# Optimization experiments

Measured on AMD Instinct MI355X. Metric: run time of the kernel, lower is better.

## Reference

```python
import jax, jax.numpy as jnp
import numpy as np

RADIUS = 0.05
HMIN = -0.02
HMAX = 0.04
NSAMPLE = 64


def setup_inputs() -> dict:
    key = jax.random.key(0)
    k1, k2, k3, k4 = jax.random.split(key, 4)
    B, N, P, C = 2, 16384, 1024, 256
    xyz = jax.random.uniform(k1, (B, N, 3), dtype=jnp.float32)
    new_xyz = jax.random.uniform(k2, (B, P, 3), dtype=jnp.float32)
    rot = jax.random.normal(k3, (B, P, 3, 3), dtype=jnp.float32)
    features = jax.random.normal(k4, (B, C, N), dtype=jnp.float32)
    return {"xyz": xyz, "new_xyz": new_xyz, "rot": rot, "features": features}


def cylinder_query(xyz, new_xyz, rot):
    """Returns (B, P, NSAMPLE) int32 indices into the N axis of xyz.

    Faithful to the torch version: the torch code sorts all N candidates by
    distance (knn with K=N) and then top-k's a cylinder score over them; since
    the candidate set is all N points, this equals a direct top-k of the score
    over N (candidate ordering only affects float ties).
    """
    # delta = candidate point - center, in world frame: (B, P, N, 3)
    delta = xyz[:, None, :, :] - new_xyz[:, :, None, :]
    # rotate into cylinder frame: matmul(delta, rot^T) -> sum_d delta_d * rot[j, d]
    dcyl = jnp.einsum('bpnd,bpjd->bpnj', delta, rot)
    x, y, z = dcyl[..., 0], dcyl[..., 1], dcyl[..., 2]
    radial = jnp.sqrt(jnp.maximum(y * y + z * z, 0.0))
    in_cyl = (radial <= RADIUS) & (x >= HMIN) & (x <= HMAX)
    score = jnp.where(in_cyl, radial + 1e-3 * jnp.abs(x), jnp.inf)
    # smallest-score top-k via top_k on negated score
    neg_vals, pos = jax.lax.top_k(-score, NSAMPLE)  # (B, P, NSAMPLE)
    vals = -neg_vals
    # fallback: nearest point (torch uses idx_cand[..., 0], the KNN-nearest)
    d2 = jnp.sum(delta * delta, axis=-1)  # (B, P, N)
    fallback = jnp.argmin(d2, axis=-1)  # (B, P)
    no_valid = jnp.isinf(vals[..., 0])  # no point inside cylinder
    idx = jnp.where(no_valid[..., None], fallback[..., None], pos)
    return idx


def reference(xyz, new_xyz, rot, features):
    B = xyz.shape[0]
    idx = cylinder_query(xyz, new_xyz, rot)  # (B, P, S)
    # group xyz: (B, P, S, 3)
    grouped_xyz = jax.vmap(lambda p, i: p[i])(xyz, idx)
    grouped_xyz = grouped_xyz - new_xyz[:, :, None, :]
    # rotate_xyz: grouped @ rot  -> sum_d g_d * rot[d, e]
    grouped_xyz = jnp.einsum('bpsd,bpde->bpse', grouped_xyz, rot)
    grouped_xyz = jnp.transpose(grouped_xyz, (0, 3, 1, 2))  # (B, 3, P, S)
    # group features: (B, C, P, S)
    grouped_feat = jax.vmap(lambda f, i: f[:, i])(features, idx)
    return jnp.concatenate([grouped_xyz, grouped_feat], axis=1)  # (B, 3+C, P, S)
```

## Files before the change

kernel.cpp:

```cpp
#include <hip/hip_runtime.h>
#include <stdint.h>

#define B_ 2
#define N_ 16384
#define P_ 1024
#define C_ 256
#define S_ 64
#define CH_ (C_ + 3)
#define CAP_ 512

#define INF_BITS 0x7F800000u

typedef unsigned long long u64;

struct QS {
    u64 keys[CAP_];
    uint32_t hist[4][256];
    u64 red[4];
    uint32_t wsum[4];
    int vflag[128];
    int cnt;
    int sel;
    uint32_t k;
};

struct GT {
    float tile[C_][33];
};

union USmem {
    QS qs;
    GT g;
};

__device__ __forceinline__ u64 umin64(u64 a, u64 b) { return a < b ? a : b; }

__device__ __forceinline__ uint32_t f2bf(float f) {
    uint32_t x = __float_as_uint(f);
    return (x + 0x7fffu + ((x >> 16) & 1u)) >> 16;
}
__device__ __forceinline__ float bf2f(uint32_t u) { return __uint_as_float(u << 16); }

__device__ u64 block_min_u64(u64 v, u64* s_red) {
    int tid = threadIdx.x;
#pragma unroll
    for (int o = 32; o > 0; o >>= 1)
        v = umin64(v, (u64)__shfl_xor(v, o, 64));
    __syncthreads();
    if ((tid & 63) == 0) s_red[tid >> 6] = v;
    __syncthreads();
    u64 r = s_red[0];
#pragma unroll
    for (int w = 1; w < 4; ++w) r = umin64(r, s_red[w]);
    return r;
}

__device__ __forceinline__ uint32_t eval_sb(float px, float py, float pz,
                                            float cx, float cy, float cz,
                                            float r0, float r1, float r2,
                                            float r3, float r4, float r5,
                                            float r6, float r7, float r8) {
    float dx = px - cx, dy = py - cy, dz = pz - cz;
    float xr = __fadd_rn(__fadd_rn(__fmul_rn(dx, r0), __fmul_rn(dy, r1)), __fmul_rn(dz, r2));
    float yr = __fadd_rn(__fadd_rn(__fmul_rn(dx, r3), __fmul_rn(dy, r4)), __fmul_rn(dz, r5));
    float zr = __fadd_rn(__fadd_rn(__fmul_rn(dx, r6), __fmul_rn(dy, r7)), __fmul_rn(dz, r8));
    float rad2 = __fadd_rn(__fmul_rn(yr, yr), __fmul_rn(zr, zr));
    float radial = __fsqrt_rn(fmaxf(rad2, 0.0f));
    bool valid = (radial <= 0.05f) && (xr >= -0.02f) && (xr <= 0.04f);
    float score = __fadd_rn(radial, __fmul_rn(1e-3f, fabsf(xr)));
    return valid ? __float_as_uint(score) : INF_BITS;
}

__device__ __forceinline__ uint32_t score_bits(const float* __restrict__ xb, int n,
                                               float cx, float cy, float cz,
                                               float r0, float r1, float r2,
                                               float r3, float r4, float r5,
                                               float r6, float r7, float r8) {
    return eval_sb(xb[n * 3 + 0], xb[n * 3 + 1], xb[n * 3 + 2],
                   cx, cy, cz, r0, r1, r2, r3, r4, r5, r6, r7, r8);
}

__device__ void select_idx(QS& qs, const float* __restrict__ xb,
                           float cx, float cy, float cz,
                           float r0, float r1, float r2, float r3, float r4,
                           float r5, float r6, float r7, float r8,
                           int* s_out) {
    const int tid = threadIdx.x;
    const int wid = tid >> 6;
    const int v = qs.cnt;

    if (v == 0) {
        u64 fb = ~0ull;
        for (int n = tid; n < N_; n += 256) {
            float px = xb[n * 3 + 0], py = xb[n * 3 + 1], pz = xb[n * 3 + 2];
            float dx = px - cx, dy = py - cy, dz = pz - cz;
            float d2 = __fadd_rn(__fadd_rn(__fmul_rn(dx, dx), __fmul_rn(dy, dy)),
                                 __fmul_rn(dz, dz));
            fb = umin64(fb, ((u64)__float_as_uint(d2) << 32) | (unsigned)n);
        }
        u64 m = block_min_u64(fb, qs.red);
        if (tid < S_) s_out[tid] = (int)(unsigned)(m & 0xFFFFFFFFu);
    } else if (v <= 64) {
        if (tid >= v && tid < 64)
            qs.keys[tid] = 0xFFFFFFFF00000000ull | (unsigned)(0x10000 + tid);
        __syncthreads();
        u64 key = 0;
        int rank = 0;
        if (tid < 64) {
            key = qs.keys[tid];
            for (int o = 0; o < 64; ++o) rank += (qs.keys[o] < key) ? 1 : 0;
        }
        __syncthreads();
        if (tid < 64) qs.keys[rank] = key;
        __syncthreads();
        const int needed = 64 - v;
        if (tid < 64 && needed > 0) {
            bool inv0 = (qs.vflag[tid] == 0);
            u64 m0 = __ballot(inv0);
            int before0 = __popcll(m0 & ((1ull << tid) - 1ull));
            if (inv0 && before0 < needed) qs.keys[v + before0] = (unsigned)tid;
            int c0 = __popcll(m0);
            if (c0 < needed) {
                bool inv1 = (qs.vflag[64 + tid] == 0);
                u64 m1 = __ballot(inv1);
                int b1 = c0 + __popcll(m1 & ((1ull << tid) - 1ull));
                if (inv1 && b1 < needed) qs.keys[v + b1] = (unsigned)(64 + tid);
            }
        }
        __syncthreads();
        if (tid < S_) s_out[tid] = (int)(unsigned)(qs.keys[tid] & 0xFFFFFFFFu);
    } else if (v <= CAP_) {
        for (int i = tid; i < v; i += 256) {
            u64 key = qs.keys[i];
            int rank = 0;
            for (int j = 0; j < v; ++j) rank += (qs.keys[j] < key) ? 1 : 0;
            if (rank < 64) s_out[rank] = (int)(unsigned)(key & 0xFFFFFFFFu);
        }
    } else {
        uint32_t prefix = 0, mask = 0, kk = 64;
        for (int pass = 0; pass < 4; ++pass) {
            const int shift = 24 - 8 * pass;
            __syncthreads();
            qs.hist[0][tid] = 0;
            qs.hist[1][tid] = 0;
            qs.hist[2][tid] = 0;
            qs.hist[3][tid] = 0;
            __syncthreads();
            for (int n = tid; n < N_; n += 256) {
                uint32_t sb = score_bits(xb, n, cx, cy, cz, r0, r1, r2, r3, r4, r5, r6, r7, r8);
                if (sb != INF_BITS && (sb & mask) == prefix)
                    atomicAdd(&qs.hist[wid][(sb >> shift) & 255u], 1u);
            }
            __syncthreads();
            uint32_t cnt = qs.hist[0][tid] + qs.hist[1][tid] + qs.hist[2][tid] + qs.hist[3][tid];
            uint32_t x = cnt;
#pragma unroll
            for (int o = 1; o < 64; o <<= 1) {
                uint32_t y = __shfl_up(x, o, 64);
                if ((tid & 63) >= o) x += y;
            }
            if ((tid & 63) == 63) qs.wsum[wid] = x;
            __syncthreads();
            uint32_t woff = 0;
            for (int w = 0; w < wid; ++w) woff += qs.wsum[w];
            uint32_t incl = x + woff;
            uint32_t excl = incl - cnt;
            if (kk > excl && kk <= incl) {
                qs.sel = tid;
                qs.k = kk - excl;
            }
            __syncthreads();
            prefix |= ((uint32_t)qs.sel) << shift;
            mask |= 255u << shift;
            kk = qs.k;
        }
        const uint32_t T = prefix;

        __syncthreads();
        if (tid == 0) qs.cnt = 0;
        __syncthreads();
        for (int n = tid; n < N_; n += 256) {
            uint32_t sb = score_bits(xb, n, cx, cy, cz, r0, r1, r2, r3, r4, r5, r6, r7, r8);
            if (sb != INF_BITS && sb <= T) {
                int pos = atomicAdd(&qs.cnt, 1);
                if (pos < CAP_) qs.keys[pos] = ((u64)sb << 32) | (unsigned)n;
            }
        }
        __syncthreads();
        int c = qs.cnt;
        if (c > CAP_) c = CAP_;
        for (int i = tid; i < c; i += 256) {
            u64 key = qs.keys[i];
            int rank = 0;
            for (int j = 0; j < c; ++j) rank += (qs.keys[j] < key) ? 1 : 0;
            if (rank < 64) s_out[rank] = (int)(unsigned)(key & 0xFFFFFFFFu);
        }
    }
}

__global__ __launch_bounds__(256) void transpose_kernel(const float* __restrict__ feat,
                                                        ushort* __restrict__ featT) {
    int t = blockIdx.x;
    int b = t >> 10;
    int rem = t & 1023;
    int cblk = rem >> 8;
    int nblk = rem & 255;
    __shared__ float tile[64][65];
    int tid = threadIdx.x;
    for (int i = tid; i < 64 * 64; i += 256) {
        int cy = i >> 6, nx = i & 63;
        tile[cy][nx] = feat[((size_t)(b * C_ + cblk * 64 + cy)) * N_ + nblk * 64 + nx];
    }
    __syncthreads();
    for (int i = tid; i < 64 * 32; i += 256) {
        int ny = i >> 5, cp = i & 31;
        uint32_t u0 = f2bf(tile[2 * cp + 0][ny]);
        uint32_t u1 = f2bf(tile[2 * cp + 1][ny]);
        *(uint32_t*)&featT[((size_t)(b * N_ + nblk * 64 + ny)) * C_ + cblk * 64 + 2 * cp] =
            u0 | (u1 << 16);
    }
}

__global__ __launch_bounds__(256) void qg_kernel(const ushort* __restrict__ featT,
                                                 const float* __restrict__ features,
                                                 const float* __restrict__ xyz,
                                                 const float* __restrict__ new_xyz,
                                                 const float* __restrict__ rot,
                                                 float* __restrict__ out, int useT) {
    __shared__ USmem sm;
    __shared__ int s_idx[S_];
    const int tid = threadIdx.x;
    const int lane = tid & 63;
    const int bp = blockIdx.x;
    const int b = bp >> 10;
    const int p = bp & 1023;

    if (tid == 0) sm.qs.cnt = 0;

    const float cx = new_xyz[bp * 3 + 0];
    const float cy = new_xyz[bp * 3 + 1];
    const float cz = new_xyz[bp * 3 + 2];
    const float* R = rot + (size_t)bp * 9;
    const float r0 = R[0], r1 = R[1], r2 = R[2];
    const float r3 = R[3], r4 = R[4], r5 = R[5];
    const float r6 = R[6], r7 = R[7], r8 = R[8];

    __syncthreads();

    const float* xb = xyz + (size_t)b * N_ * 3;
    const float4* xb4 = (const float4*)xb;

    for (int it = 0; it < N_ / 1024; ++it) {
        int t4 = it * 256 + tid;
        float4 A = xb4[t4 * 3 + 0];
        float4 Bv = xb4[t4 * 3 + 1];
        float4 Cv = xb4[t4 * 3 + 2];
        int n0 = t4 * 4;

        uint32_t s0 = eval_sb(A.x, A.y, A.z, cx, cy, cz, r0, r1, r2, r3, r4, r5, r6, r7, r8);
        uint32_t s1 = eval_sb(A.w, Bv.x, Bv.y, cx, cy, cz, r0, r1, r2, r3, r4, r5, r6, r7, r8);
        uint32_t s2 = eval_sb(Bv.z, Bv.w, Cv.x, cx, cy, cz, r0, r1, r2, r3, r4, r5, r6, r7, r8);
        uint32_t s3 = eval_sb(Cv.y, Cv.z, Cv.w, cx, cy, cz, r0, r1, r2, r3, r4, r5, r6, r7, r8);

        if (it == 0 && tid < 32) {
            sm.qs.vflag[n0 + 0] = (s0 != INF_BITS) ? 1 : 0;
            sm.qs.vflag[n0 + 1] = (s1 != INF_BITS) ? 1 : 0;
            sm.qs.vflag[n0 + 2] = (s2 != INF_BITS) ? 1 : 0;
            sm.qs.vflag[n0 + 3] = (s3 != INF_BITS) ? 1 : 0;
        }
        uint32_t mn = min(min(s0, s1), min(s2, s3));
        if (__any(mn != INF_BITS)) {
            uint32_t sb[4] = {s0, s1, s2, s3};
#pragma unroll
            for (int j = 0; j < 4; ++j) {
                u64 m = __ballot(sb[j] != INF_BITS);
                if (m) {
                    int leader = __builtin_ctzll(m);
                    int cnt = __popcll(m);
                    int base = 0;
                    if (lane == leader) base = atomicAdd(&sm.qs.cnt, cnt);
                    base = __shfl(base, leader, 64);
                    if (sb[j] != INF_BITS) {
                        int pos = base + __popcll(m & ((1ull << lane) - 1ull));
                        if (pos < CAP_) sm.qs.keys[pos] = ((u64)sb[j] << 32) | (unsigned)(n0 + j);
                    }
                }
            }
        }
    }
    __syncthreads();

    select_idx(sm.qs, xb, cx, cy, cz, r0, r1, r2, r3, r4, r5, r6, r7, r8, s_idx);
    __syncthreads();

    if (tid < S_) {
        int n = s_idx[tid];
        const float* pt = xyz + ((size_t)b * N_ + n) * 3;
        float dx = pt[0] - cx;
        float dy = pt[1] - cy;
        float dz = pt[2] - cz;
        float g0 = __fadd_rn(__fadd_rn(__fmul_rn(dx, r0), __fmul_rn(dy, r3)), __fmul_rn(dz, r6));
        float g1 = __fadd_rn(__fadd_rn(__fmul_rn(dx, r1), __fmul_rn(dy, r4)), __fmul_rn(dz, r7));
        float g2 = __fadd_rn(__fadd_rn(__fmul_rn(dx, r2), __fmul_rn(dy, r5)), __fmul_rn(dz, r8));
        out[(((size_t)b * CH_ + 0) * P_ + p) * S_ + tid] = g0;
        out[(((size_t)b * CH_ + 1) * P_ + p) * S_ + tid] = g1;
        out[(((size_t)b * CH_ + 2) * P_ + p) * S_ + tid] = g2;
    }

    for (int h = 0; h < 2; ++h) {
        if (h) __syncthreads();
        if (useT) {
            for (int i = tid; i < 32 * 128; i += 256) {
                int sl = i >> 7, cp = i & 127;
                int n = s_idx[h * 32 + sl];
                uint32_t v = *(const uint32_t*)&featT[((size_t)b * N_ + n) * C_ + cp * 2];
                sm.g.tile[2 * cp + 0][sl] = bf2f(v & 0xffffu);
                sm.g.tile[2 * cp + 1][sl] = bf2f(v >> 16);
            }
        } else {
            for (int i = tid; i < 32 * C_; i += 256) {
                int sl = i >> 8;
                int n = s_idx[h * 32 + sl];
                sm.g.tile[tid][sl] = features[((size_t)b * C_ + tid) * N_ + n];
            }
        }
        __syncthreads();
        for (int i = tid; i < C_ * 8; i += 256) {
            int c = i >> 3, s4 = (i & 7) * 4;
            float4 v;
            v.x = sm.g.tile[c][s4 + 0];
            v.y = sm.g.tile[c][s4 + 1];
            v.z = sm.g.tile[c][s4 + 2];
            v.w = sm.g.tile[c][s4 + 3];
            *(float4*)&out[(((size_t)b * CH_ + 3 + c) * P_ + p) * S_ + h * 32 + s4] = v;
        }
    }
}

extern "C" void kernel_launch(void* const* d_in, const int* in_sizes, int n_in,
                              void* d_out, int out_size, void* d_ws, size_t ws_size,
                              hipStream_t stream) {
    const float* xyz = (const float*)d_in[0];
    const float* new_xyz = (const float*)d_in[1];
    const float* rot = (const float*)d_in[2];
    const float* features = (const float*)d_in[3];
    float* out = (float*)d_out;

    const size_t featT_bytes = (size_t)B_ * N_ * C_ * sizeof(ushort);
    const int useT = (ws_size >= featT_bytes) ? 1 : 0;

    ushort* featT = (ushort*)d_ws;

    if (useT) {
        transpose_kernel<<<2048, 256, 0, stream>>>(features, featT);
    }
    qg_kernel<<<B_ * P_, 256, 0, stream>>>(featT, features, xyz, new_xyz, rot, out, useT);
}
```

Before: 74.06 us.

## Split query and feature gather; stage full feature rows in LDS

Drops the bf16 transpose pre-pass and the per-query feature gather. The query kernel now writes the selected indices to workspace, and a new group kernel takes one (batch, channel) row per block. That kernel loads the full 16384-float row into shared memory (64 KB), gathers every query's samples from LDS and writes them as coalesced float4 stores. This removes the transposed bf16 copy along with its precision loss and the strided gathers. It costs a second launch, a global index round-trip, and large shared memory per block, which limits occupancy.

```diff
diff --git a/kernel.cpp b/kernel.cpp
--- a/kernel.cpp
+++ b/kernel.cpp
@@ -24,22 +24,7 @@
     uint32_t k;
 };
 
-struct GT {
-    float tile[C_][33];
-};
-
-union USmem {
-    QS qs;
-    GT g;
-};
-
 __device__ __forceinline__ u64 umin64(u64 a, u64 b) { return a < b ? a : b; }
-
-__device__ __forceinline__ uint32_t f2bf(float f) {
-    uint32_t x = __float_as_uint(f);
-    return (x + 0x7fffu + ((x >> 16) & 1u)) >> 16;
-}
-__device__ __forceinline__ float bf2f(uint32_t u) { return __uint_as_float(u << 16); }
 
 __device__ u64 block_min_u64(u64 v, u64* s_red) {
     int tid = threadIdx.x;
@@ -198,36 +183,12 @@
     }
 }
 
-__global__ __launch_bounds__(256) void transpose_kernel(const float* __restrict__ feat,
-                                                        ushort* __restrict__ featT) {
-    int t = blockIdx.x;
-    int b = t >> 10;
-    int rem = t & 1023;
-    int cblk = rem >> 8;
-    int nblk = rem & 255;
-    __shared__ float tile[64][65];
-    int tid = threadIdx.x;
-    for (int i = tid; i < 64 * 64; i += 256) {
-        int cy = i >> 6, nx = i & 63;
-        tile[cy][nx] = feat[((size_t)(b * C_ + cblk * 64 + cy)) * N_ + nblk * 64 + nx];
-    }
-    __syncthreads();
-    for (int i = tid; i < 64 * 32; i += 256) {
-        int ny = i >> 5, cp = i & 31;
-        uint32_t u0 = f2bf(tile[2 * cp + 0][ny]);
-        uint32_t u1 = f2bf(tile[2 * cp + 1][ny]);
-        *(uint32_t*)&featT[((size_t)(b * N_ + nblk * 64 + ny)) * C_ + cblk * 64 + 2 * cp] =
-            u0 | (u1 << 16);
-    }
-}
-
-__global__ __launch_bounds__(256) void qg_kernel(const ushort* __restrict__ featT,
-                                                 const float* __restrict__ features,
-                                                 const float* __restrict__ xyz,
-                                                 const float* __restrict__ new_xyz,
-                                                 const float* __restrict__ rot,
-                                                 float* __restrict__ out, int useT) {
-    __shared__ USmem sm;
+__global__ __launch_bounds__(256) void query_kernel(const float* __restrict__ xyz,
+                                                    const float* __restrict__ new_xyz,
+                                                    const float* __restrict__ rot,
+                                                    int* __restrict__ idx_out,
+                                                    float* __restrict__ out) {
+    __shared__ QS qs;
     __shared__ int s_idx[S_];
     const int tid = threadIdx.x;
     const int lane = tid & 63;
@@ -235,7 +196,7 @@
     const int b = bp >> 10;
     const int p = bp & 1023;
 
-    if (tid == 0) sm.qs.cnt = 0;
+    if (tid == 0) qs.cnt = 0;
 
     const float cx = new_xyz[bp * 3 + 0];
     const float cy = new_xyz[bp * 3 + 1];
@@ -263,10 +224,10 @@
         uint32_t s3 = eval_sb(Cv.y, Cv.z, Cv.w, cx, cy, cz, r0, r1, r2, r3, r4, r5, r6, r7, r8);
 
         if (it == 0 && tid < 32) {
-            sm.qs.vflag[n0 + 0] = (s0 != INF_BITS) ? 1 : 0;
-            sm.qs.vflag[n0 + 1] = (s1 != INF_BITS) ? 1 : 0;
-            sm.qs.vflag[n0 + 2] = (s2 != INF_BITS) ? 1 : 0;
-            sm.qs.vflag[n0 + 3] = (s3 != INF_BITS) ? 1 : 0;
+            qs.vflag[n0 + 0] = (s0 != INF_BITS) ? 1 : 0;
+            qs.vflag[n0 + 1] = (s1 != INF_BITS) ? 1 : 0;
+            qs.vflag[n0 + 2] = (s2 != INF_BITS) ? 1 : 0;
+            qs.vflag[n0 + 3] = (s3 != INF_BITS) ? 1 : 0;
         }
         uint32_t mn = min(min(s0, s1), min(s2, s3));
         if (__any(mn != INF_BITS)) {
@@ -278,11 +239,11 @@
                     int leader = __builtin_ctzll(m);
                     int cnt = __popcll(m);
                     int base = 0;
-                    if (lane == leader) base = atomicAdd(&sm.qs.cnt, cnt);
+                    if (lane == leader) base = atomicAdd(&qs.cnt, cnt);
                     base = __shfl(base, leader, 64);
                     if (sb[j] != INF_BITS) {
                         int pos = base + __popcll(m & ((1ull << lane) - 1ull));
-                        if (pos < CAP_) sm.qs.keys[pos] = ((u64)sb[j] << 32) | (unsigned)(n0 + j);
+                        if (pos < CAP_) qs.keys[pos] = ((u64)sb[j] << 32) | (unsigned)(n0 + j);
                     }
                 }
             }
@@ -290,11 +251,12 @@
     }
     __syncthreads();
 
-    select_idx(sm.qs, xb, cx, cy, cz, r0, r1, r2, r3, r4, r5, r6, r7, r8, s_idx);
+    select_idx(qs, xb, cx, cy, cz, r0, r1, r2, r3, r4, r5, r6, r7, r8, s_idx);
     __syncthreads();
 
     if (tid < S_) {
         int n = s_idx[tid];
+        idx_out[(size_t)bp * S_ + tid] = n;
         const float* pt = xyz + ((size_t)b * N_ + n) * 3;
         float dx = pt[0] - cx;
         float dy = pt[1] - cy;
@@ -306,34 +268,35 @@
         out[(((size_t)b * CH_ + 1) * P_ + p) * S_ + tid] = g1;
         out[(((size_t)b * CH_ + 2) * P_ + p) * S_ + tid] = g2;
     }
-
-    for (int h = 0; h < 2; ++h) {
-        if (h) __syncthreads();
-        if (useT) {
-            for (int i = tid; i < 32 * 128; i += 256) {
-                int sl = i >> 7, cp = i & 127;
-                int n = s_idx[h * 32 + sl];
-                uint32_t v = *(const uint32_t*)&featT[((size_t)b * N_ + n) * C_ + cp * 2];
-                sm.g.tile[2 * cp + 0][sl] = bf2f(v & 0xffffu);
-                sm.g.tile[2 * cp + 1][sl] = bf2f(v >> 16);
-            }
-        } else {
-            for (int i = tid; i < 32 * C_; i += 256) {
-                int sl = i >> 8;
-                int n = s_idx[h * 32 + sl];
-                sm.g.tile[tid][sl] = features[((size_t)b * C_ + tid) * N_ + n];
-            }
-        }
-        __syncthreads();
-        for (int i = tid; i < C_ * 8; i += 256) {
-            int c = i >> 3, s4 = (i & 7) * 4;
-            float4 v;
-            v.x = sm.g.tile[c][s4 + 0];
-            v.y = sm.g.tile[c][s4 + 1];
-            v.z = sm.g.tile[c][s4 + 2];
-            v.w = sm.g.tile[c][s4 + 3];
-            *(float4*)&out[(((size_t)b * CH_ + 3 + c) * P_ + p) * S_ + h * 32 + s4] = v;
-        }
+}
+
+__global__ __launch_bounds__(256) void group_kernel(const float* __restrict__ features,
+                                                    const int* __restrict__ idx,
+                                                    float* __restrict__ out) {
+    __shared__ float row[N_];
+    const int tid = threadIdx.x;
+    const int bc = blockIdx.x;
+    const int b = bc >> 8;
+    const int c = bc & 255;
+
+    const float4* src = (const float4*)(features + (size_t)bc * N_);
+    for (int i = tid; i < N_ / 4; i += 256) {
+        float4 v = src[i];
+        *(float4*)&row[i * 4] = v;
+    }
+    __syncthreads();
+
+    const int4* idx4 = (const int4*)(idx + (size_t)b * P_ * S_);
+    float* outc = out + ((size_t)b * CH_ + 3 + c) * P_ * S_;
+#pragma unroll 4
+    for (int i = tid; i < P_ * (S_ / 4); i += 256) {
+        int4 id = idx4[i];
+        float4 v;
+        v.x = row[id.x];
+        v.y = row[id.y];
+        v.z = row[id.z];
+        v.w = row[id.w];
+        *(float4*)&outc[(size_t)i * 4] = v;
     }
 }
 
@@ -346,13 +309,8 @@
     const float* features = (const float*)d_in[3];
     float* out = (float*)d_out;
 
-    const size_t featT_bytes = (size_t)B_ * N_ * C_ * sizeof(ushort);
-    const int useT = (ws_size >= featT_bytes) ? 1 : 0;
-
-    ushort* featT = (ushort*)d_ws;
-
-    if (useT) {
-        transpose_kernel<<<2048, 256, 0, stream>>>(features, featT);
-    }
-    qg_kernel<<<B_ * P_, 256, 0, stream>>>(featT, features, xyz, new_xyz, rot, out, useT);
-}
+    int* idx = (int*)d_ws;
+
+    query_kernel<<<B_ * P_, 256, 0, stream>>>(xyz, new_xyz, rot, idx, out);
+    group_kernel<<<B_ * C_, 256, 0, stream>>>(features, idx, out);
+}
```

Result: slower. 95.38 us (+28.8%).
